# Optimization experiments

Measured on AMD Instinct MI355X. Metric: run time of the kernel, lower is better.

The kernel has to match this reference:

```python
import jax, jax.numpy as jnp
import numpy as np

RADIUS = 1.0 / 16.0
MAX_NEIGHBORS = 64  # forward() passes max_num_neighbors=64
N_POINTS = 16384
N_CLOUDS = 8


def _radius_neighbors(pos, batch, r, k):
    """Dense radius graph: for each point, up to k in-radius same-cloud neighbors.
    Returns idx [N,k] int32 and mask [N,k] bool. loop=True -> self always valid."""
    sq = jnp.sum(pos * pos, axis=-1)                        # [N]
    d2 = sq[:, None] + sq[None, :] - 2.0 * (pos @ pos.T)    # [N,N]
    d2 = jnp.maximum(d2, 0.0)
    valid = (d2 <= r * r) & (batch[:, None] == batch[None, :])
    score = jnp.where(valid, -d2, -jnp.inf)
    vals, idx = jax.lax.top_k(score, k)                     # nearest-first, [N,k]
    mask = vals > -jnp.inf
    return idx, mask


def _point_conv(x, pos, idx, mask, W1, b1, W2, b2):
    """PointNetConv: msg = relu(Linear([x_j, pos_j - pos_i])), max-agg, Linear."""
    xj = x[idx]                                   # [N,K,c_in]  gather
    rel = pos[idx] - pos[:, None, :]              # [N,K,3]
    h = jnp.concatenate([xj, rel], axis=-1) @ W1 + b1   # [N,K,c_mid]
    h = jax.nn.relu(h)
    h = jnp.where(mask[..., None], h, -jnp.inf)
    agg = jnp.max(h, axis=1)                      # [N,c_mid]  max aggregation
    agg = jnp.where(jnp.isfinite(agg), agg, 0.0)  # safety (loop=True makes this moot)
    return agg @ W2 + b2                          # [N,c_out]


def setup_inputs() -> dict:
    key = jax.random.key(0)
    ks = jax.random.split(key, 16)
    pos = jax.random.uniform(ks[0], (N_POINTS, 3), dtype=jnp.float32)
    rgb = jax.random.uniform(ks[1], (N_POINTS, 3), dtype=jnp.float32)
    batch = jnp.sort(jax.random.randint(ks[2], (N_POINTS,), 0, N_CLOUDS)).astype(jnp.int64)

    def lin(k, fan_in, fan_out):
        kw, kb = jax.random.split(k)
        bound = 1.0 / np.sqrt(fan_in)
        W = jax.random.uniform(kw, (fan_in, fan_out), jnp.float32, -bound, bound)
        b = jax.random.uniform(kb, (fan_out,), jnp.float32, -bound, bound)
        return W, b

    W1a, b1a = lin(ks[3], 3 + 3, 8)
    W2a, b2a = lin(ks[4], 8, 8)
    W1b, b1b = lin(ks[5], 8 + 3, 16)
    W2b, b2b = lin(ks[6], 16, 16)
    W1c, b1c = lin(ks[7], 16 + 3, 32)
    W2c, b2c = lin(ks[8], 32, 32)
    return {"pos": pos, "rgb": rgb, "batch": batch,
            "W1a": W1a, "b1a": b1a, "W2a": W2a, "b2a": b2a,
            "W1b": W1b, "b1b": b1b, "W2b": W2b, "b2b": b2b,
            "W1c": W1c, "b1c": b1c, "W2c": W2c, "b2c": b2c}


def reference(pos, rgb, batch,
              W1a, b1a, W2a, b2a,
              W1b, b1b, W2b, b2b,
              W1c, b1c, W2c, b2c):
    # NOTE: rgb is accepted by the original forward() but never used.
    idx, mask = _radius_neighbors(pos, batch, RADIUS, MAX_NEIGHBORS)
    out = jax.nn.celu(_point_conv(pos, pos, idx, mask, W1a, b1a, W2a, b2a))
    out = jax.nn.celu(_point_conv(out, pos, idx, mask, W1b, b1b, W2b, b2b))
    out = jax.nn.celu(_point_conv(out, pos, idx, mask, W1c, b1c, W2c, b2c))
    return pos, out, batch
```

## Files before the change

### kernel.cpp

```cpp
#include <hip/hip_runtime.h>
#include <math.h>

#define N_POINTS 16384
#define CELLS_PER_CLOUD 4096
#define N_CELLS 32768
#define CAP 16
#define NBR_STRIDE 32

constexpr double R2D = 1.0 / 256.0;

__device__ int g_cnt[N_CELLS];

__global__ __launch_bounds__(256) void k_prep(const float* __restrict__ pos,
                                              const int* __restrict__ batch,
                                              float* __restrict__ out,
                                              float4* __restrict__ bucket,
                                              float4* __restrict__ pos4)
{
    int i = blockIdx.x * 256 + threadIdx.x;
    out[i]                = pos[i];
    out[i + N_POINTS]     = pos[i + N_POINTS];
    out[i + 2 * N_POINTS] = pos[i + 2 * N_POINTS];
    out[3 * N_POINTS + 32 * N_POINTS + i] = (float)batch[i];

    float x = pos[3 * i], y = pos[3 * i + 1], z = pos[3 * i + 2];
    int ix = min(max((int)(x * 16.f), 0), 15);
    int iy = min(max((int)(y * 16.f), 0), 15);
    int iz = min(max((int)(z * 16.f), 0), 15);
    int cell = ((batch[i] * 16 + iz) * 16 + iy) * 16 + ix;
    pos4[i] = make_float4(x, y, z, __int_as_float(cell));
    int slot = atomicAdd(&g_cnt[cell], 1);
    if (slot < CAP) bucket[cell * CAP + slot] = make_float4(x, y, z, __int_as_float(i));
}

__global__ __launch_bounds__(256) void k_search_a(
    const float4* __restrict__ pos4, const float4* __restrict__ bucket,
    const float* __restrict__ W1, const float* __restrict__ b1,
    const float* __restrict__ W2, const float* __restrict__ b2,
    float* __restrict__ out_a, float4* __restrict__ nbr, int* __restrict__ nbr_cnt)
{
    __shared__ float sW1[48], sB1[8], sW2[64], sB2[8];
    __shared__ float4 s_hits[NBR_STRIDE][8];
    __shared__ int   s_k[8];
    __shared__ float s_mx[8][9];

    int t = threadIdx.x;
    int p = t >> 5;
    int g = t & 31;

    if (t < 48) sW1[t] = W1[t];
    if (t < 8) { sB1[t] = b1[t]; sB2[t] = b2[t]; s_k[t] = 0; }
    if (t < 64) sW2[t] = W2[t];
    __syncthreads();

    int i = blockIdx.x * 8 + p;
    float4 pi4 = pos4[i];
    float xi = pi4.x, yi = pi4.y, zi = pi4.z;
    double xd = (double)xi, yd = (double)yi, zd = (double)zi;
    int cell0 = __float_as_int(pi4.w);
    int ix = cell0 & 15, iy = (cell0 >> 4) & 15, iz = (cell0 >> 8) & 15;
    int cb = cell0 & ~(CELLS_PER_CLOUD - 1);

    int dz = g / 9 - 1, dy = (g / 3) % 3 - 1, dx = g % 3 - 1;
    int zz = iz + dz, yy = iy + dy, xx = ix + dx;
    bool ok = (g < 27) & ((zz | yy | xx) >= 0) & (zz < 16) & (yy < 16) & (xx < 16);
    int zc = min(max(zz, 0), 15), yc = min(max(yy, 0), 15),
        xc = min(max(xx, 0), 15);
    int cid = cb + (zc << 8) + (yc << 4) + xc;
    int nc = min(g_cnt[cid], CAP);
    int n = ok ? nc : 0;

    for (int s = 0; s < n; s++) {
        float4 q = bucket[cid * CAP + s];
        double ddx = xd - (double)q.x, ddy = yd - (double)q.y,
               ddz = zd - (double)q.z;
        double d2 = ddx * ddx + ddy * ddy + ddz * ddz;
        if (d2 <= R2D) {
            int slot = atomicAdd(&s_k[p], 1);
            if (slot < NBR_STRIDE) {
                s_hits[slot][p] = q;
                nbr[i * NBR_STRIDE + slot] = q;
            }
        }
    }
    __syncthreads();
    int kc = min(s_k[p], NBR_STRIDE);

    if (g == 0) nbr_cnt[i] = kc;

    if (g < 8) {
        float mxv = 0.f;
        for (int kk = 0; kk < kc; kk++) {
            float4 q = s_hits[kk][p];
            float in6[6] = { q.x, q.y, q.z, q.x - xi, q.y - yi, q.z - zi };
            float h = sB1[g];
#pragma unroll
            for (int c6 = 0; c6 < 6; c6++) h = fmaf(in6[c6], sW1[c6 * 8 + g], h);
            mxv = fmaxf(mxv, fmaxf(h, 0.f));
        }
        s_mx[p][g] = mxv;
    }
    __syncthreads();
    if (g < 8) {
        float o = sB2[g];
#pragma unroll
        for (int k = 0; k < 8; k++) o = fmaf(s_mx[p][k], sW2[k * 8 + g], o);
        out_a[i * 8 + g] = o > 0.f ? o : expm1f(o);
    }
}

template<int CIN4, int CMID, int PTS, bool ZERO_CNT>
__global__ __launch_bounds__(256) void k_conv(
    const float4* __restrict__ pos4, const float4* __restrict__ xin4,
    const float4* __restrict__ nbr, const int* __restrict__ nbr_cnt,
    const float* __restrict__ W1, const float* __restrict__ b1,
    const float* __restrict__ W2, const float* __restrict__ b2,
    float* __restrict__ xout)
{
    constexpr int CIN = CIN4 * 4;
    __shared__ float4 s_q[PTS][NBR_STRIDE];
    __shared__ float4 s_x[PTS][NBR_STRIDE][CIN4];
    __shared__ float  s_agg[PTS][CMID + 1];

    int tid = threadIdx.x;

    if (ZERO_CNT) {
        int gid = blockIdx.x * 256 + tid;
        if (gid < N_CELLS) g_cnt[gid] = 0;
    }

#pragma unroll
    for (int w = tid; w < PTS * NBR_STRIDE; w += 256) {
        int sp = w >> 5, slot = w & 31;
        int si = blockIdx.x * PTS + sp;
        if (slot < nbr_cnt[si]) {
            float4 q = nbr[si * NBR_STRIDE + slot];
            s_q[sp][slot] = q;
            int j = __float_as_int(q.w);
#pragma unroll
            for (int k = 0; k < CIN4; k++) s_x[sp][slot][k] = xin4[j * CIN4 + k];
        }
    }
    __syncthreads();

    int p = tid / CMID;
    int m = tid % CMID;
    int i = blockIdx.x * PTS + p;

    float4 pi = pos4[i];
    int cnt = nbr_cnt[i];

    float w1c[CIN + 3];
#pragma unroll
    for (int k = 0; k < CIN + 3; k++) w1c[k] = W1[k * CMID + m];
    float w2c[CMID];
#pragma unroll
    for (int k = 0; k < CMID; k++) w2c[k] = W2[k * CMID + m];
    float bb = b1[m];

    float mxv = 0.f;
    for (int t = 0; t < cnt; t++) {
        float4 q = s_q[p][t];
        float h = bb;
#pragma unroll
        for (int k = 0; k < CIN4; k++) {
            float4 v = s_x[p][t][k];
            h = fmaf(v.x, w1c[4 * k],     h);
            h = fmaf(v.y, w1c[4 * k + 1], h);
            h = fmaf(v.z, w1c[4 * k + 2], h);
            h = fmaf(v.w, w1c[4 * k + 3], h);
        }
        h = fmaf(q.x - pi.x, w1c[CIN],     h);
        h = fmaf(q.y - pi.y, w1c[CIN + 1], h);
        h = fmaf(q.z - pi.z, w1c[CIN + 2], h);
        mxv = fmaxf(mxv, fmaxf(h, 0.f));
    }
    s_agg[p][m] = mxv;
    __syncthreads();

    float o = b2[m];
#pragma unroll
    for (int k = 0; k < CMID; k++) o = fmaf(s_agg[p][k], w2c[k], o);
    xout[i * CMID + m] = o > 0.f ? o : expm1f(o);
}

extern "C" void kernel_launch(void* const* d_in, const int* in_sizes, int n_in,
                              void* d_out, int out_size, void* d_ws, size_t ws_size,
                              hipStream_t stream)
{
    const float* pos   = (const float*)d_in[0];
    const int*   batch = (const int*)d_in[2];
    const float* W1a = (const float*)d_in[3];
    const float* b1a = (const float*)d_in[4];
    const float* W2a = (const float*)d_in[5];
    const float* b2a = (const float*)d_in[6];
    const float* W1b = (const float*)d_in[7];
    const float* b1b = (const float*)d_in[8];
    const float* W2b = (const float*)d_in[9];
    const float* b2b = (const float*)d_in[10];
    const float* W1c = (const float*)d_in[11];
    const float* b1c = (const float*)d_in[12];
    const float* W2c = (const float*)d_in[13];
    const float* b2c = (const float*)d_in[14];

    float* out = (float*)d_out;

    char* ws = (char*)d_ws;
    size_t off = 0;
    auto alloc = [&](size_t bytes) {
        char* p = ws + off; off += (bytes + 255) & ~size_t(255); return p;
    };
    float4* bucket  = (float4*)alloc((size_t)N_CELLS * CAP * 16);
    float4* pos4    = (float4*)alloc(N_POINTS * 16);
    int*    nbr_cnt = (int*)alloc(N_POINTS * 4);
    float4* nbr     = (float4*)alloc((size_t)N_POINTS * NBR_STRIDE * 16);
    float*  out_a   = (float*)alloc(N_POINTS * 8 * 4);
    float*  out_b   = (float*)alloc(N_POINTS * 16 * 4);

    hipLaunchKernelGGL(k_prep, dim3(N_POINTS / 256), dim3(256), 0, stream,
                       pos, batch, out, bucket, pos4);
    hipLaunchKernelGGL(k_search_a, dim3(N_POINTS / 8), dim3(256), 0, stream,
                       pos4, bucket, W1a, b1a, W2a, b2a,
                       out_a, nbr, nbr_cnt);
    hipLaunchKernelGGL((k_conv<2, 16, 16, false>), dim3(N_POINTS / 16), dim3(256), 0, stream,
                       pos4, (const float4*)out_a, nbr, nbr_cnt,
                       W1b, b1b, W2b, b2b, out_b);
    hipLaunchKernelGGL((k_conv<4, 32, 8, true>), dim3(N_POINTS / 8), dim3(256), 0, stream,
                       pos4, (const float4*)out_b, nbr, nbr_cnt,
                       W1c, b1c, W2c, b2c, out + 3 * N_POINTS);
}
```

Measured before the change: 110.5 us.

## Fuse conv layers b and c into one kernel with halo recompute

Merges the second and third point-conv kernels into a single kernel. Each block recomputes layer-b features for every neighbor of its 8 points, batching neighbor entries 16 at a time, and stores them in shared memory, so the out_b round-trip through global memory and one launch go away. The cost is redundant work: layer b is recomputed roughly once per neighbor edge (about the average neighbor count times) and needs extra gathers and syncs.

Result: slower. 121.2 us (+9.7%).

```diff
diff --git a/kernel.cpp b/kernel.cpp
--- a/kernel.cpp
+++ b/kernel.cpp
@@ -109,79 +109,154 @@
     }
 }
 
-template<int CIN4, int CMID, int PTS, bool ZERO_CNT>
-__global__ __launch_bounds__(256) void k_conv(
-    const float4* __restrict__ pos4, const float4* __restrict__ xin4,
+__global__ __launch_bounds__(256) void k_conv_bc(
+    const float4* __restrict__ pos4, const float4* __restrict__ out_a4,
     const float4* __restrict__ nbr, const int* __restrict__ nbr_cnt,
-    const float* __restrict__ W1, const float* __restrict__ b1,
-    const float* __restrict__ W2, const float* __restrict__ b2,
-    float* __restrict__ xout)
+    const float* __restrict__ W1b, const float* __restrict__ b1b,
+    const float* __restrict__ W2b, const float* __restrict__ b2b,
+    const float* __restrict__ W1c, const float* __restrict__ b1c,
+    const float* __restrict__ W2c, const float* __restrict__ b2c,
+    float* __restrict__ out)
 {
-    constexpr int CIN = CIN4 * 4;
-    __shared__ float4 s_q[PTS][NBR_STRIDE];
-    __shared__ float4 s_x[PTS][NBR_STRIDE][CIN4];
-    __shared__ float  s_agg[PTS][CMID + 1];
+    __shared__ float4 s_q[8][NBR_STRIDE];
+    __shared__ int    s_cnt[8], s_base[9], s_ent[256];
+    __shared__ float4 s_bq[16][NBR_STRIDE];
+    __shared__ float4 s_ba[16][NBR_STRIDE][2];
+    __shared__ float  s_gag[16][17];
+    __shared__ float  s_b[8][NBR_STRIDE][16];
+    __shared__ float  s_aggc[8][33];
 
     int tid = threadIdx.x;
 
-    if (ZERO_CNT) {
-        int gid = blockIdx.x * 256 + tid;
-        if (gid < N_CELLS) g_cnt[gid] = 0;
-    }
-
-#pragma unroll
-    for (int w = tid; w < PTS * NBR_STRIDE; w += 256) {
-        int sp = w >> 5, slot = w & 31;
-        int si = blockIdx.x * PTS + sp;
-        if (slot < nbr_cnt[si]) {
-            float4 q = nbr[si * NBR_STRIDE + slot];
-            s_q[sp][slot] = q;
-            int j = __float_as_int(q.w);
-#pragma unroll
-            for (int k = 0; k < CIN4; k++) s_x[sp][slot][k] = xin4[j * CIN4 + k];
-        }
-    }
-    __syncthreads();
-
-    int p = tid / CMID;
-    int m = tid % CMID;
-    int i = blockIdx.x * PTS + p;
-
-    float4 pi = pos4[i];
-    int cnt = nbr_cnt[i];
-
-    float w1c[CIN + 3];
-#pragma unroll
-    for (int k = 0; k < CIN + 3; k++) w1c[k] = W1[k * CMID + m];
-    float w2c[CMID];
-#pragma unroll
-    for (int k = 0; k < CMID; k++) w2c[k] = W2[k * CMID + m];
-    float bb = b1[m];
+    if (blockIdx.x < N_CELLS / 256) g_cnt[blockIdx.x * 256 + tid] = 0;
+
+    int p8 = tid >> 5, sl = tid & 31;
+    int ip = blockIdx.x * 8 + p8;
+    if (sl == 0) s_cnt[p8] = nbr_cnt[ip];
+    s_q[p8][sl] = nbr[ip * NBR_STRIDE + sl];
+    __syncthreads();
+    if (tid == 0) {
+        int a = 0;
+#pragma unroll
+        for (int pp = 0; pp < 8; pp++) { s_base[pp] = a; a += s_cnt[pp]; }
+        s_base[8] = a;
+    }
+    __syncthreads();
+    if (sl < s_cnt[p8]) s_ent[s_base[p8] + sl] = (p8 << 8) | sl;
+    __syncthreads();
+    int L = s_base[8];
+
+    int lane_e = tid >> 4;
+    int me     = tid & 15;
+    float wb1[11], wb2[16];
+#pragma unroll
+    for (int k = 0; k < 11; k++) wb1[k] = W1b[k * 16 + me];
+#pragma unroll
+    for (int k = 0; k < 16; k++) wb2[k] = W2b[k * 16 + me];
+    float bb1 = b1b[me], bb2 = b2b[me];
+
+    for (int eb = 0; eb < L; eb += 16) {
+        int e = eb + lane_e;
+        bool act = e < L;
+        int pp = 0, ss = 0, j = 0, cj = 0;
+        float4 qj = make_float4(0.f, 0.f, 0.f, 0.f);
+        if (act) {
+            int en = s_ent[e];
+            pp = en >> 8; ss = en & 255;
+            qj = s_q[pp][ss];
+            j = __float_as_int(qj.w);
+            cj = nbr_cnt[j];
+        }
+#pragma unroll
+        for (int h2 = 0; h2 < 2; h2++) {
+            int kk = me + 16 * h2;
+            if (act && kk < cj) {
+                float4 qk = nbr[j * NBR_STRIDE + kk];
+                s_bq[lane_e][kk] = qk;
+                int kidx = __float_as_int(qk.w);
+                s_ba[lane_e][kk][0] = out_a4[kidx * 2];
+                s_ba[lane_e][kk][1] = out_a4[kidx * 2 + 1];
+            }
+        }
+        __syncthreads();
+        float mx = 0.f;
+        if (act) {
+            float xj = qj.x, yj = qj.y, zj = qj.z;
+            for (int kk = 0; kk < cj; kk++) {
+                float4 v0 = s_ba[lane_e][kk][0], v1 = s_ba[lane_e][kk][1];
+                float4 qk = s_bq[lane_e][kk];
+                float h = bb1;
+                h = fmaf(v0.x, wb1[0], h);
+                h = fmaf(v0.y, wb1[1], h);
+                h = fmaf(v0.z, wb1[2], h);
+                h = fmaf(v0.w, wb1[3], h);
+                h = fmaf(v1.x, wb1[4], h);
+                h = fmaf(v1.y, wb1[5], h);
+                h = fmaf(v1.z, wb1[6], h);
+                h = fmaf(v1.w, wb1[7], h);
+                h = fmaf(qk.x - xj, wb1[8],  h);
+                h = fmaf(qk.y - yj, wb1[9],  h);
+                h = fmaf(qk.z - zj, wb1[10], h);
+                mx = fmaxf(mx, fmaxf(h, 0.f));
+            }
+        }
+        s_gag[lane_e][me] = mx;
+        __syncthreads();
+        if (act) {
+            float o = bb2;
+#pragma unroll
+            for (int k = 0; k < 16; k++) o = fmaf(s_gag[lane_e][k], wb2[k], o);
+            o = o > 0.f ? o : expm1f(o);
+            s_b[pp][ss][me] = o;
+        }
+        __syncthreads();
+    }
+
+    int pc = tid >> 5, mc = tid & 31;
+    int ic = blockIdx.x * 8 + pc;
+    float4 pic = pos4[ic];
+    int cntc = s_cnt[pc];
+    float w1r[19], w2r[32];
+#pragma unroll
+    for (int k = 0; k < 19; k++) w1r[k] = W1c[k * 32 + mc];
+#pragma unroll
+    for (int k = 0; k < 32; k++) w2r[k] = W2c[k * 32 + mc];
+    float bbc = b1c[mc];
 
     float mxv = 0.f;
-    for (int t = 0; t < cnt; t++) {
-        float4 q = s_q[p][t];
-        float h = bb;
-#pragma unroll
-        for (int k = 0; k < CIN4; k++) {
-            float4 v = s_x[p][t][k];
-            h = fmaf(v.x, w1c[4 * k],     h);
-            h = fmaf(v.y, w1c[4 * k + 1], h);
-            h = fmaf(v.z, w1c[4 * k + 2], h);
-            h = fmaf(v.w, w1c[4 * k + 3], h);
-        }
-        h = fmaf(q.x - pi.x, w1c[CIN],     h);
-        h = fmaf(q.y - pi.y, w1c[CIN + 1], h);
-        h = fmaf(q.z - pi.z, w1c[CIN + 2], h);
+    for (int tt = 0; tt < cntc; tt++) {
+        float4 q = s_q[pc][tt];
+        const float4* fb4 = (const float4*)&s_b[pc][tt][0];
+        float4 f0 = fb4[0], f1 = fb4[1], f2 = fb4[2], f3 = fb4[3];
+        float h = bbc;
+        h = fmaf(f0.x, w1r[0],  h);
+        h = fmaf(f0.y, w1r[1],  h);
+        h = fmaf(f0.z, w1r[2],  h);
+        h = fmaf(f0.w, w1r[3],  h);
+        h = fmaf(f1.x, w1r[4],  h);
+        h = fmaf(f1.y, w1r[5],  h);
+        h = fmaf(f1.z, w1r[6],  h);
+        h = fmaf(f1.w, w1r[7],  h);
+        h = fmaf(f2.x, w1r[8],  h);
+        h = fmaf(f2.y, w1r[9],  h);
+        h = fmaf(f2.z, w1r[10], h);
+        h = fmaf(f2.w, w1r[11], h);
+        h = fmaf(f3.x, w1r[12], h);
+        h = fmaf(f3.y, w1r[13], h);
+        h = fmaf(f3.z, w1r[14], h);
+        h = fmaf(f3.w, w1r[15], h);
+        h = fmaf(q.x - pic.x, w1r[16], h);
+        h = fmaf(q.y - pic.y, w1r[17], h);
+        h = fmaf(q.z - pic.z, w1r[18], h);
         mxv = fmaxf(mxv, fmaxf(h, 0.f));
     }
-    s_agg[p][m] = mxv;
-    __syncthreads();
-
-    float o = b2[m];
-#pragma unroll
-    for (int k = 0; k < CMID; k++) o = fmaf(s_agg[p][k], w2c[k], o);
-    xout[i * CMID + m] = o > 0.f ? o : expm1f(o);
+    s_aggc[pc][mc] = mxv;
+    __syncthreads();
+
+    float o = b2c[mc];
+#pragma unroll
+    for (int k = 0; k < 32; k++) o = fmaf(s_aggc[pc][k], w2r[k], o);
+    out[3 * N_POINTS + ic * 32 + mc] = o > 0.f ? o : expm1f(o);
 }
 
 extern "C" void kernel_launch(void* const* d_in, const int* in_sizes, int n_in,
@@ -215,17 +290,13 @@
     int*    nbr_cnt = (int*)alloc(N_POINTS * 4);
     float4* nbr     = (float4*)alloc((size_t)N_POINTS * NBR_STRIDE * 16);
     float*  out_a   = (float*)alloc(N_POINTS * 8 * 4);
-    float*  out_b   = (float*)alloc(N_POINTS * 16 * 4);
 
     hipLaunchKernelGGL(k_prep, dim3(N_POINTS / 256), dim3(256), 0, stream,
                        pos, batch, out, bucket, pos4);
     hipLaunchKernelGGL(k_search_a, dim3(N_POINTS / 8), dim3(256), 0, stream,
                        pos4, bucket, W1a, b1a, W2a, b2a,
                        out_a, nbr, nbr_cnt);
-    hipLaunchKernelGGL((k_conv<2, 16, 16, false>), dim3(N_POINTS / 16), dim3(256), 0, stream,
+    hipLaunchKernelGGL(k_conv_bc, dim3(N_POINTS / 8), dim3(256), 0, stream,
                        pos4, (const float4*)out_a, nbr, nbr_cnt,
-                       W1b, b1b, W2b, b2b, out_b);
-    hipLaunchKernelGGL((k_conv<4, 32, 8, true>), dim3(N_POINTS / 8), dim3(256), 0, stream,
-                       pos4, (const float4*)out_b, nbr, nbr_cnt,
-                       W1c, b1c, W2c, b2c, out + 3 * N_POINTS);
+                       W1b, b1b, W2b, b2b, W1c, b1c, W2c, b2c, out);
 }
```
